# Performance work log

Measured on AMD Instinct MI355X. Metric: run time of the kernel, lower is better.

## Reference

```python
import jax, jax.numpy as jnp
import numpy as np

T, HEADS, DIM_HEAD = 16, 16, 72
M = HEADS * DIM_HEAD  # 1152
SCALE = DIM_HEAD ** -0.5


def _ln(x, eps):
    mu = x.mean(-1, keepdims=True)
    var = x.var(-1, keepdims=True)
    return (x - mu) / jnp.sqrt(var + eps)


def _rotate_half(t):
    # interleaved pairs (x1, x2) -> (-x2, x1), as in rotary-embedding-torch
    t1, t2 = t[..., 0::2], t[..., 1::2]
    return jnp.stack([-t2, t1], axis=-1).reshape(t.shape)


def _rotary(t, pos):
    d = t.shape[-1]
    inv_freq = 1.0 / (10000.0 ** (jnp.arange(0, d, 2, dtype=jnp.float32) / d))
    freqs = pos.astype(jnp.float32)[:, None] * inv_freq          # (T, d/2)
    freqs = jnp.repeat(freqs, 2, axis=-1)                        # (T, d)
    return t * jnp.cos(freqs) + _rotate_half(t) * jnp.sin(freqs)


def _forward(x, c4t, c, W_ada, b_ada, tn_w, tn_b, t_qkv, t_k, t_v, t_out,
             t_fc_w, t_fc_b, s_qkv, s_k, s_v, s_out,
             mlp_w1, mlp_b1, mlp_w2, mlp_b2, f):
    B = c4t.shape[0]
    K, N, _ = x.shape

    ada = jax.nn.silu(c4t) @ W_ada + b_ada                       # (B, 6M)
    sh_msa, sc_msa, g_msa, sh_mlp, sc_mlp, g_mlp = jnp.split(ada, 6, axis=1)

    x4 = x.reshape(B, T, N, M)

    # ---- temporal attention (seq dim = frames, rotary, per-frame cond k/v) ----
    xt = _ln(x4, 1e-5) * tn_w + tn_b                             # temporal_norm1
    xt = xt.transpose(0, 2, 1, 3)                                # (B, N, T, M)
    q, k, v = jnp.split(xt @ t_qkv, 3, axis=-1)

    def heads_t(t):  # (B,N,T,M) -> (B,N,h,T,d)
        return t.reshape(B, N, T, HEADS, DIM_HEAD).transpose(0, 1, 3, 2, 4)

    q, k, v = map(heads_t, (q, k, v))
    k = _rotary(k, f)
    ek = (c @ t_k).reshape(B, T, HEADS, DIM_HEAD).transpose(0, 2, 1, 3)  # (B,h,T,d)
    ev = (c @ t_v).reshape(B, T, HEADS, DIM_HEAD).transpose(0, 2, 1, 3)
    ek = _rotary(ek, f)
    ek = jnp.broadcast_to(ek[:, None], k.shape)                  # (B,N,h,T,d)
    ev = jnp.broadcast_to(ev[:, None], v.shape)
    kk = jnp.concatenate([ek, k], axis=-2)                       # (B,N,h,2T,d)
    vv = jnp.concatenate([ev, v], axis=-2)
    q = _rotary(q * SCALE, f)
    attn = jax.nn.softmax(jnp.einsum('bnhid,bnhjd->bnhij', q, kk), axis=-1)
    out = jnp.einsum('bnhij,bnhjd->bnhid', attn, vv)
    out = out.transpose(0, 1, 3, 2, 4).reshape(B, N, T, M) @ t_out
    res = out.transpose(0, 2, 1, 3) @ t_fc_w + t_fc_b            # (B,T,N,M)
    x4 = x4 + res

    # ---- spatial attention with adaLN modulate + one cond token per frame ----
    mod = _ln(x4, 1e-6) * (1.0 + sc_msa[:, None, None, :]) + sh_msa[:, None, None, :]
    q, k, v = jnp.split(mod @ s_qkv, 3, axis=-1)

    def heads_s(t):  # (B,T,N,M) -> (B,T,h,N,d)
        return t.reshape(B, T, N, HEADS, DIM_HEAD).transpose(0, 1, 3, 2, 4)

    q, k, v = map(heads_s, (q, k, v))
    ek = (c @ s_k).reshape(B, T, HEADS, DIM_HEAD)[:, :, :, None, :]  # (B,T,h,1,d)
    ev = (c @ s_v).reshape(B, T, HEADS, DIM_HEAD)[:, :, :, None, :]
    kk = jnp.concatenate([ek, k], axis=-2)                       # (B,T,h,N+1,d)
    vv = jnp.concatenate([ev, v], axis=-2)
    attn = jax.nn.softmax(jnp.einsum('bthid,bthjd->bthij', q * SCALE, kk), axis=-1)
    out = jnp.einsum('bthij,bthjd->bthid', attn, vv)
    out = out.transpose(0, 1, 3, 2, 4).reshape(B, T, N, M) @ s_out
    x4 = x4 + g_msa[:, None, None, :] * out

    # ---- gated MLP with adaLN modulate ----
    mod2 = _ln(x4, 1e-6) * (1.0 + sc_mlp[:, None, None, :]) + sh_mlp[:, None, None, :]
    h = jax.nn.gelu(mod2 @ mlp_w1 + mlp_b1, approximate=True)
    y = h @ mlp_w2 + mlp_b2
    x4 = x4 + g_mlp[:, None, None, :] * y
    return x4.reshape(K, N, M)


def setup_inputs() -> dict:
    key = jax.random.key(0)
    ks = jax.random.split(key, 20)
    B, N = 2, 256

    def w(k, shape, s=0.02):
        return jax.random.normal(k, shape, jnp.float32) * s

    return {
        'x': jax.random.normal(ks[0], (B * T, N, M), jnp.float32),
        'c4t': jax.random.normal(ks[1], (B, M), jnp.float32),
        'c': jax.random.normal(ks[2], (B, T, M), jnp.float32),
        'W_ada': w(ks[3], (M, 6 * M)), 'b_ada': w(ks[4], (6 * M,)),
        'tn_w': jnp.ones(M, jnp.float32), 'tn_b': jnp.zeros(M, jnp.float32),
        't_qkv': w(ks[5], (M, 3 * M)), 't_k': w(ks[6], (M, M)),
        't_v': w(ks[7], (M, M)), 't_out': w(ks[8], (M, M)),
        't_fc_w': w(ks[9], (M, M)), 't_fc_b': jnp.zeros(M, jnp.float32),
        's_qkv': w(ks[10], (M, 3 * M)), 's_k': w(ks[11], (M, M)),
        's_v': w(ks[12], (M, M)), 's_out': w(ks[13], (M, M)),
        'mlp_w1': w(ks[14], (M, 4 * M)), 'mlp_b1': jnp.zeros(4 * M, jnp.float32),
        'mlp_w2': w(ks[15], (4 * M, M)), 'mlp_b2': jnp.zeros(M, jnp.float32),
        'f': jnp.arange(T, dtype=jnp.int32),
    }


def reference(x, c4t, c, W_ada, b_ada, tn_w, tn_b, t_qkv, t_k, t_v, t_out,
              t_fc_w, t_fc_b, s_qkv, s_k, s_v, s_out,
              mlp_w1, mlp_b1, mlp_w2, mlp_b2, f):
    return _forward(x, c4t, c, W_ada, b_ada, tn_w, tn_b, t_qkv, t_k, t_v, t_out,
                    t_fc_w, t_fc_b, s_qkv, s_k, s_v, s_out,
                    mlp_w1, mlp_b1, mlp_w2, mlp_b2, f)
```

## Files before the change

### kernel.cpp

```cpp
#include <hip/hip_runtime.h>
#include <hip/hip_bf16.h>

typedef __hip_bfloat16 bf16;
typedef __attribute__((ext_vector_type(8))) short short8;
typedef __attribute__((ext_vector_type(4))) float floatx4;

__device__ __forceinline__ float b2f(bf16 v) { return __bfloat162float(v); }
__device__ __forceinline__ short f2bs(float v) {
    bf16 h = __float2bfloat16(v);
    return *(short*)&h;
}
__device__ __forceinline__ float invfreq(int jj) {
    return expf(-0.25584278811044955f * (float)jj);
}

template<int MODE>
__device__ __forceinline__ float ldin(const void* p, long i) {
    if (MODE == 0) return b2f(((const bf16*)p)[i]);
    else           return ((const float*)p)[i];
}

#define SCALE_ 0.11785113019775793f

#define GLDS(gp, lp) __builtin_amdgcn_global_load_lds( \
    (const __attribute__((address_space(1))) void*)(gp), \
    (__attribute__((address_space(3))) void*)(lp), 16, 0, 0)

__global__ void k_detect(const void* __restrict__ x, int* __restrict__ flag)
{
    const unsigned short* u = (const unsigned short*)x;
    int tid = threadIdx.x;
    int insane = 0;
    for (int i = tid; i < 2048; i += 64) {
        unsigned short s = u[i];
        int ex = (s >> 7) & 0xFF;
        if (ex >= 0xC5) insane++;
    }
    #pragma unroll
    for (int off = 32; off > 0; off >>= 1) insane += __shfl_down(insane, off);
    if (tid == 0) flag[0] = (insane > 8) ? 1 : 0;
}

__global__ void k_rope(const int* __restrict__ f, float* __restrict__ ropeC,
                       float* __restrict__ ropeS)
{
    int idx = blockIdx.x * 256 + threadIdx.x;
    if (idx < 1152) {
        int t = idx / 72, d = idx - t * 72;
        float ang = (float)f[t] * invfreq(d >> 1);
        float sn, cs; sincosf(ang, &sn, &cs);
        ropeC[idx] = cs;
        ropeS[idx] = sn;
    }
}

__global__ void k_silu(const void* __restrict__ c4t, float* __restrict__ out,
                       const int* __restrict__ flg)
{
    int i = blockIdx.x * 256 + threadIdx.x;
    if (i < 2304) {
        float v = (*flg == 0) ? ldin<0>(c4t, i) : ldin<1>(c4t, i);
        out[i] = v / (1.f + expf(-v));
    }
}

__global__ void k_cvt(const void* __restrict__ in, float* __restrict__ out, int n,
                      const int* __restrict__ flg)
{
    int i = blockIdx.x * 256 + threadIdx.x;
    if (i < n) out[i] = (*flg == 0) ? ldin<0>(in, i) : ldin<1>(in, i);
}

__global__ void k_cvtb(const float* __restrict__ in, bf16* __restrict__ out, int n)
{
    int i = blockIdx.x * 256 + threadIdx.x;
    if (i < n) out[i] = __float2bfloat16(in[i]);
}

template<int MODE>
__device__ __forceinline__ void wt_body(float (*tile)[33], const void* __restrict__ W,
    bf16* __restrict__ Wt, int K, int N)
{
    int n0 = blockIdx.x << 5, k0 = blockIdx.y << 5;
    int tid = threadIdx.x;
    int r = tid >> 3, c4 = (tid & 7) << 2;
    long base = (long)(k0 + r) * N + n0 + c4;
    #pragma unroll
    for (int i = 0; i < 4; ++i) tile[r][c4 + i] = ldin<MODE>(W, base + i);
    __syncthreads();
    long obase = (long)(n0 + r) * K + k0 + c4;
    #pragma unroll
    for (int i = 0; i < 4; ++i) Wt[obase + i] = __float2bfloat16(tile[c4 + i][r]);
}

__global__ __launch_bounds__(256) void k_wt(const void* __restrict__ W,
    bf16* __restrict__ Wt, int K, int N, const int* __restrict__ flg)
{
    __shared__ float tile[32][33];
    if (*flg == 0) wt_body<0>(tile, W, Wt, K, N);
    else           wt_body<1>(tile, W, Wt, K, N);
}

template<int MODE>
__device__ __forceinline__ void gemm_body(
    float (*As)[64], float (*Bs)[64],
    const float* __restrict__ A, const void* __restrict__ W,
    const void* __restrict__ bias, float* __restrict__ C,
    int R, int K, int N)
{
    int tid = threadIdx.x;
    int tx = tid & 15, ty = tid >> 4;
    int row0 = blockIdx.y << 6;
    int col0 = blockIdx.x << 6;
    float acc[4][4] = {};
    int ar = tid >> 2;
    int ak = (tid & 3) << 2;
    int bk = tid >> 4;
    int bc = (tid & 15) << 2;
    for (int kt = 0; kt < K; kt += 16) {
        if (row0 + ar < R) {
            const float4 a4 = *(const float4*)(A + (long)(row0 + ar) * K + kt + ak);
            As[ak + 0][ar] = a4.x; As[ak + 1][ar] = a4.y;
            As[ak + 2][ar] = a4.z; As[ak + 3][ar] = a4.w;
        } else {
            As[ak + 0][ar] = 0.f; As[ak + 1][ar] = 0.f;
            As[ak + 2][ar] = 0.f; As[ak + 3][ar] = 0.f;
        }
        #pragma unroll
        for (int i = 0; i < 4; ++i)
            Bs[bk][bc + i] = ldin<MODE>(W, (long)(kt + bk) * N + col0 + bc + i);
        __syncthreads();
        #pragma unroll
        for (int kk = 0; kk < 16; ++kk) {
            float4 av = *(const float4*)&As[kk][ty << 2];
            float4 bv = *(const float4*)&Bs[kk][tx << 2];
            float a[4] = {av.x, av.y, av.z, av.w};
            float b[4] = {bv.x, bv.y, bv.z, bv.w};
            #pragma unroll
            for (int i = 0; i < 4; ++i)
                #pragma unroll
                for (int j = 0; j < 4; ++j)
                    acc[i][j] += a[i] * b[j];
        }
        __syncthreads();
    }
    #pragma unroll
    for (int i = 0; i < 4; ++i) {
        int gr = row0 + (ty << 2) + i;
        if (gr >= R) continue;
        float* cp = C + (long)gr * N + col0 + (tx << 2);
        #pragma unroll
        for (int j = 0; j < 4; ++j) {
            float v = acc[i][j];
            if (bias) v += ldin<MODE>(bias, col0 + (tx << 2) + j);
            cp[j] = v;
        }
    }
}

__global__ __launch_bounds__(256) void k_gemm(
    const float* __restrict__ A, const void* __restrict__ W,
    const void* __restrict__ bias, float* __restrict__ C,
    int R, int K, int N, const int* __restrict__ flg)
{
    __shared__ float As[16][64];
    __shared__ float Bs[16][64];
    if (*flg == 0) gemm_body<0>(As, Bs, A, W, bias, C, R, K, N);
    else           gemm_body<1>(As, Bs, A, W, bias, C, R, K, N);
}

template<int EMODE>
__global__ __launch_bounds__(256) void k_mgemm(
    const bf16* __restrict__ A, const bf16* __restrict__ Wt,
    const float* __restrict__ bias, void* __restrict__ Cout,
    int K, int N, int outbf, int act,
    float* __restrict__ x4, const float* __restrict__ ada, int part,
    const void* __restrict__ xin, void* __restrict__ outp,
    const int* __restrict__ flg)
{
    __shared__ short As[8192];
    __shared__ short Bs[8192];
    int tid = threadIdx.x;
    int lane = tid & 63, wave = tid >> 6;
    int mq = wave >> 1, nq = wave & 1;

    int gx = gridDim.x;
    int nwg = gx * (int)gridDim.y;
    int orig = blockIdx.y * gx + blockIdx.x;
    int qq = nwg >> 3, rr = nwg & 7;
    int xcd = orig & 7, loc = orig >> 3;
    int wg = (xcd < rr ? xcd * (qq + 1) : rr * (qq + 1) + (xcd - rr) * qq) + loc;
    int bx = wg % gx, by = wg / gx;

    long row0 = (long)by << 7;
    long col0 = (long)bx << 7;
    int mi = lane & 15, q = lane >> 4;

    const bf16* gA0 = A  + (row0 + (2 * wave) * 16 + mi) * K + q * 8;
    const bf16* gA1 = A  + (row0 + (2 * wave + 1) * 16 + mi) * K + q * 8;
    const bf16* gB0 = Wt + (col0 + (2 * wave) * 16 + mi) * K + q * 8;
    const bf16* gB1 = Wt + (col0 + (2 * wave + 1) * 16 + mi) * K + q * 8;
    int la0 = (2 * wave) << 9;
    int la1 = (2 * wave + 1) << 9;

    floatx4 acc[4][4] = {};

    int nt = K >> 5;
    GLDS(gA0, &As[la0]);
    GLDS(gA1, &As[la1]);
    GLDS(gB0, &Bs[la0]);
    GLDS(gB1, &Bs[la1]);
    __syncthreads();

    for (int t = 0; t < nt - 1; ++t) {
        int cur = (t & 1) << 12, nxt = cur ^ 4096;
        int kt2 = (t + 1) << 5;
        GLDS(gA0 + kt2, &As[nxt + la0]);
        GLDS(gA1 + kt2, &As[nxt + la1]);
        GLDS(gB0 + kt2, &Bs[nxt + la0]);
        GLDS(gB1 + kt2, &Bs[nxt + la1]);
        short8 af[4], bfr[4];
        #pragma unroll
        for (int i = 0; i < 4; ++i)
            af[i] = *(const short8*)&As[cur + ((4 * mq + i) << 9) + lane * 8];
        #pragma unroll
        for (int j = 0; j < 4; ++j)
            bfr[j] = *(const short8*)&Bs[cur + ((4 * nq + j) << 9) + lane * 8];
        #pragma unroll
        for (int i = 0; i < 4; ++i)
            #pragma unroll
            for (int j = 0; j < 4; ++j)
                acc[i][j] = __builtin_amdgcn_mfma_f32_16x16x32_bf16(
                    af[i], bfr[j], acc[i][j], 0, 0, 0);
        __syncthreads();
    }
    {
        int cur = ((nt - 1) & 1) << 12;
        short8 af[4], bfr[4];
        #pragma unroll
        for (int i = 0; i < 4; ++i)
            af[i] = *(const short8*)&As[cur + ((4 * mq + i) << 9) + lane * 8];
        #pragma unroll
        for (int j = 0; j < 4; ++j)
            bfr[j] = *(const short8*)&Bs[cur + ((4 * nq + j) << 9) + lane * 8];
        #pragma unroll
        for (int i = 0; i < 4; ++i)
            #pragma unroll
            for (int j = 0; j < 4; ++j)
                acc[i][j] = __builtin_amdgcn_mfma_f32_16x16x32_bf16(
                    af[i], bfr[j], acc[i][j], 0, 0, 0);
    }

    int lr = lane >> 4, lc = lane & 15;
    int fl = flg ? *flg : 0;
    float b4[4] = {0.f, 0.f, 0.f, 0.f};
    if (bias) {
        #pragma unroll
        for (int j = 0; j < 4; ++j) b4[j] = bias[(int)col0 + nq * 64 + j * 16 + lc];
    }
    #pragma unroll
    for (int i = 0; i < 4; ++i) {
        #pragma unroll
        for (int r = 0; r < 4; ++r) {
            long grow = row0 + mq * 64 + i * 16 + lr * 4 + r;
            #pragma unroll
            for (int j = 0; j < 4; ++j) {
                int col = (int)col0 + nq * 64 + j * 16 + lc;
                float v = acc[i][j][r] + b4[j];
                if (act) {
                    float u = v;
                    float tt = 1.5957691216057308f * (u + 0.044715f * u * u * u);
                    v = u / (1.f + __expf(-tt));
                }
                if constexpr (EMODE == 0) {
                    if (outbf) ((bf16*)Cout)[grow * N + col] = __float2bfloat16(v);
                    else       ((float*)Cout)[grow * N + col] = v;
                } else if constexpr (EMODE == 1) {
                    int bb = (int)(grow >> 12);
                    int nn = ((int)grow >> 4) & 255;
                    int tt2 = (int)grow & 15;
                    long rx = ((long)((bb << 4) + tt2) << 8) + nn;
                    long idx = rx * 1152 + col;
                    float xv = (fl == 0) ? b2f(((const bf16*)xin)[idx])
                                         : ((const float*)xin)[idx];
                    x4[idx] = xv + v;
                } else {
                    int bb = (int)(grow >> 12);
                    float g = ada[(bb * 6 + part) * 1152 + col];
                    long idx = grow * 1152 + col;
                    float nv = x4[idx] + g * v;
                    x4[idx] = nv;
                    if (outp) {
                        if (fl == 0) ((bf16*)outp)[idx] = __float2bfloat16(nv);
                        else         ((float*)outp)[idx] = nv;
                    }
                }
            }
        }
    }
}

template<int MODE>
__device__ __forceinline__ void ln_t_body(float* rs, float* rss,
    const void* __restrict__ x, const void* __restrict__ w,
    const void* __restrict__ bb, bf16* __restrict__ out)
{
    int r = blockIdx.x;
    int n = r & 255;
    int bt = r >> 8;
    int b = bt >> 4, t = bt & 15;
    long orow = (long)((b << 8) + n) * 16 + t;
    int tid = threadIdx.x;
    float vals[5];
    float s = 0.f, ss = 0.f;
    int c = 0;
    for (int i = tid; i < 1152; i += 256, ++c) {
        float v = ldin<MODE>(x, (long)r * 1152 + i);
        vals[c] = v; s += v; ss += v * v;
    }
    #pragma unroll
    for (int off = 32; off > 0; off >>= 1) {
        s  += __shfl_down(s, off);
        ss += __shfl_down(ss, off);
    }
    int wid = tid >> 6;
    if ((tid & 63) == 0) { rs[wid] = s; rss[wid] = ss; }
    __syncthreads();
    float S  = rs[0] + rs[1] + rs[2] + rs[3];
    float SS = rss[0] + rss[1] + rss[2] + rss[3];
    float mu = S * (1.f / 1152.f);
    float var = SS * (1.f / 1152.f) - mu * mu;
    float rstd = rsqrtf(var + 1e-5f);
    c = 0;
    bf16* op = out + orow * 1152;
    for (int i = tid; i < 1152; i += 256, ++c)
        op[i] = __float2bfloat16((vals[c] - mu) * rstd * ldin<MODE>(w, i) + ldin<MODE>(bb, i));
}

__global__ __launch_bounds__(256) void k_ln_t(
    const void* __restrict__ x, const void* __restrict__ w,
    const void* __restrict__ bb, bf16* __restrict__ out,
    const int* __restrict__ flg)
{
    __shared__ float rs[4], rss[4];
    if (*flg == 0) ln_t_body<0>(rs, rss, x, w, bb, out);
    else           ln_t_body<1>(rs, rss, x, w, bb, out);
}

__global__ __launch_bounds__(256) void k_ln_mod(
    const float* __restrict__ x4, const float* __restrict__ ada,
    int psh, int psc, float eps, bf16* __restrict__ out)
{
    int r = blockIdx.x;
    int b = r >> 12;
    const float* xp = x4 + (long)r * 1152;
    int tid = threadIdx.x;
    float vals[5];
    float s = 0.f, ss = 0.f;
    int c = 0;
    for (int i = tid; i < 1152; i += 256, ++c) {
        float v = xp[i];
        vals[c] = v; s += v; ss += v * v;
    }
    #pragma unroll
    for (int off = 32; off > 0; off >>= 1) {
        s  += __shfl_down(s, off);
        ss += __shfl_down(ss, off);
    }
    __shared__ float rs[4], rss[4];
    int wid = tid >> 6;
    if ((tid & 63) == 0) { rs[wid] = s; rss[wid] = ss; }
    __syncthreads();
    float S  = rs[0] + rs[1] + rs[2] + rs[3];
    float SS = rss[0] + rss[1] + rss[2] + rss[3];
    float mu = S * (1.f / 1152.f);
    float var = SS * (1.f / 1152.f) - mu * mu;
    float rstd = rsqrtf(var + eps);
    const float* sh = ada + (b * 6 + psh) * 1152;
    const float* sc = ada + (b * 6 + psc) * 1152;
    c = 0;
    bf16* op = out + (long)r * 1152;
    for (int i = tid; i < 1152; i += 256, ++c)
        op[i] = __float2bfloat16((vals[c] - mu) * rstd * (1.f + sc[i]) + sh[i]);
}

__global__ __launch_bounds__(256) void k_attn_t(
    const bf16* __restrict__ qkv, const float* __restrict__ ekt,
    const float* __restrict__ evt, const float* __restrict__ ropeC,
    const float* __restrict__ ropeS, bf16* __restrict__ out)
{
    __shared__ float qs[16][73];
    __shared__ float ksT[72][33];
    __shared__ float vs[32][73];
    __shared__ float sc[16][33];
    int blk = blockIdx.x;
    int h = blk & 15;
    int bn = blk >> 4;
    int b = bn >> 8;
    int tid = threadIdx.x;
    long qbase = (long)bn * 16 * 3456 + h * 72;
    for (int idx = tid; idx < 16 * 72; idx += 256) {
        int i = idx / 72, d = idx - i * 72;
        long p0 = qbase + (long)i * 3456;
        float v  = b2f(qkv[p0 + d]);
        float v2 = b2f(qkv[p0 + (d ^ 1)]);
        float cs = ropeC[idx], sn = ropeS[idx];
        float rv = (d & 1) ? (v * cs + v2 * sn) : (v * cs - v2 * sn);
        qs[i][d] = rv * SCALE_;
    }
    for (int idx = tid; idx < 32 * 72; idx += 256) {
        int j = idx / 72, d = idx - j * 72;
        float kv, kv2, vv; int pi;
        if (j < 16) {
            long base = (long)(b * 16 + j) * 1152 + h * 72;
            kv  = ekt[base + d];
            kv2 = ekt[base + (d ^ 1)];
            vv  = evt[base + d];
            pi = j;
        } else {
            int jj = j - 16;
            long base = qbase + (long)jj * 3456;
            kv  = b2f(qkv[base + 1152 + d]);
            kv2 = b2f(qkv[base + 1152 + (d ^ 1)]);
            vv  = b2f(qkv[base + 2304 + d]);
            pi = jj;
        }
        float cs = ropeC[pi * 72 + d], sn = ropeS[pi * 72 + d];
        ksT[d][j] = (d & 1) ? (kv * cs + kv2 * sn) : (kv * cs - kv2 * sn);
        vs[j][d] = vv;
    }
    __syncthreads();
    for (int e = tid; e < 512; e += 256) {
        int i = e >> 5, j = e & 31;
        float s = 0.f;
        for (int d = 0; d < 72; ++d) s += qs[i][d] * ksT[d][j];
        sc[i][j] = s;
    }
    __syncthreads();
    if (tid < 16) {
        float m = -1e30f;
        for (int j = 0; j < 32; ++j) m = fmaxf(m, sc[tid][j]);
        float l = 0.f;
        for (int j = 0; j < 32; ++j) { float p = expf(sc[tid][j] - m); sc[tid][j] = p; l += p; }
        float inv = 1.f / l;
        for (int j = 0; j < 32; ++j) sc[tid][j] *= inv;
    }
    __syncthreads();
    for (int idx = tid; idx < 16 * 72; idx += 256) {
        int i = idx / 72, d = idx - i * 72;
        float o = 0.f;
        for (int j = 0; j < 32; ++j) o += sc[i][j] * vs[j][d];
        out[((long)bn * 16 + i) * 1152 + h * 72 + d] = __float2bfloat16(o);
    }
}

__global__ __launch_bounds__(256) void k_attn_s(
    const bf16* __restrict__ qkv, const bf16* __restrict__ eksb,
    const bf16* __restrict__ evsb, bf16* __restrict__ out)
{
    __shared__ short vT[5120];
    __shared__ short pl[4][1024];
    int tid = threadIdx.x;
    int lane = tid & 63, wave = tid >> 6;
    int blk = blockIdx.x;
    int ic = blk & 3;
    int bth = blk >> 2;
    int h = bth & 15;
    int bt = bth >> 4;
    int col = lane & 15, q = lane >> 4;
    int hoff = h * 72;
    long qkvbase = (long)bt * 256 * 3456;
    long ctxbase = (long)bt * 1152 + hoff;

    int qrow = ic * 64 + wave * 16 + col;
    const bf16* qptr = qkv + qkvbase + (long)qrow * 3456 + hoff;
    short8 qf[3];
    #pragma unroll
    for (int ks = 0; ks < 3; ++ks) {
        int k0 = ks * 32 + q * 8;
        if (k0 + 8 <= 72) qf[ks] = *(const short8*)(qptr + k0);
        else { short8 z = {0,0,0,0,0,0,0,0}; qf[ks] = z; }
    }

    floatx4 o[5] = {};
    float m_i[4], l_i[4];
    #pragma unroll
    for (int r = 0; r < 4; ++r) { m_i[r] = -1e30f; l_i[r] = 0.f; }

    for (int kc = 0; kc < 320; kc += 64) {
        for (int fi = tid; fi < 640; fi += 256) {
            int blkid = fi >> 6, fl2 = fi & 63;
            int dn = blkid >> 1, ks = blkid & 1;
            int d = dn * 16 + (fl2 & 15);
            int kq = fl2 >> 4;
            short8 v;
            #pragma unroll
            for (int j = 0; j < 8; ++j) {
                int gk = kc + ks * 32 + kq * 8 + j;
                short sv = 0;
                if (d < 72 && gk <= 256) {
                    if (gk == 0) sv = *(const short*)(eksb ? &evsb[ctxbase + d] : nullptr);
                    else sv = *(const short*)&qkv[qkvbase + (long)(gk - 1) * 3456 + 2304 + hoff + d];
                }
                v[j] = sv;
            }
            *(short8*)&vT[blkid * 512 + fl2 * 8] = v;
        }
        __syncthreads();

        floatx4 sacc[4] = {};
        #pragma unroll
        for (int nt = 0; nt < 4; ++nt) {
            int key = kc + nt * 16 + col;
            #pragma unroll
            for (int ks = 0; ks < 3; ++ks) {
                int k0 = ks * 32 + q * 8;
                short8 kf = {0,0,0,0,0,0,0,0};
                if (key <= 256 && k0 + 8 <= 72) {
                    if (key == 0) kf = *(const short8*)(eksb + ctxbase + k0);
                    else kf = *(const short8*)(qkv + qkvbase + (long)(key - 1) * 3456 + 1152 + hoff + k0);
                }
                sacc[nt] = __builtin_amdgcn_mfma_f32_16x16x32_bf16(qf[ks], kf, sacc[nt], 0, 0, 0);
            }
        }

        float p[4][4];
        #pragma unroll
        for (int r = 0; r < 4; ++r) {
            float mv = -1e30f;
            #pragma unroll
            for (int nt = 0; nt < 4; ++nt) {
                int key = kc + nt * 16 + col;
                float s = (key <= 256) ? sacc[nt][r] * SCALE_ : -1e30f;
                p[nt][r] = s;
                mv = fmaxf(mv, s);
            }
            #pragma unroll
            for (int xm = 1; xm < 16; xm <<= 1) mv = fmaxf(mv, __shfl_xor(mv, xm));
            float mn = fmaxf(m_i[r], mv);
            float alpha = expf(m_i[r] - mn);
            m_i[r] = mn;
            float rsum = 0.f;
            #pragma unroll
            for (int nt = 0; nt < 4; ++nt) {
                float e = expf(p[nt][r] - mn);
                p[nt][r] = e;
                rsum += e;
            }
            #pragma unroll
            for (int xm = 1; xm < 16; xm <<= 1) rsum += __shfl_xor(rsum, xm);
            l_i[r] = l_i[r] * alpha + rsum;
            #pragma unroll
            for (int dn = 0; dn < 5; ++dn) o[dn][r] *= alpha;
        }

        #pragma unroll
        for (int nt = 0; nt < 4; ++nt) {
            int kl = nt * 16 + col;
            int ks2 = kl >> 5, q2 = (kl >> 3) & 3, j = kl & 7;
            #pragma unroll
            for (int r = 0; r < 4; ++r) {
                int mrow = q * 4 + r;
                pl[wave][ks2 * 512 + q2 * 128 + mrow * 8 + j] = f2bs(p[nt][r]);
            }
        }
        __syncthreads();

        #pragma unroll
        for (int ks = 0; ks < 2; ++ks) {
            short8 pf = *(const short8*)&pl[wave][ks * 512 + lane * 8];
            #pragma unroll
            for (int dn = 0; dn < 5; ++dn) {
                short8 vf = *(const short8*)&vT[(dn * 2 + ks) * 512 + lane * 8];
                o[dn] = __builtin_amdgcn_mfma_f32_16x16x32_bf16(pf, vf, o[dn], 0, 0, 0);
            }
        }
        __syncthreads();
    }

    int orow0 = ic * 64 + wave * 16;
    #pragma unroll
    for (int dn = 0; dn < 5; ++dn) {
        int d = dn * 16 + col;
        if (d >= 72) continue;
        #pragma unroll
        for (int r = 0; r < 4; ++r) {
            int mrow = q * 4 + r;
            float val = o[dn][r] / l_i[r];
            out[((long)bt * 256 + orow0 + mrow) * 1152 + hoff + d] = __float2bfloat16(val);
        }
    }
}

extern "C" void kernel_launch(void* const* d_in, const int* in_sizes, int n_in,
                              void* d_out, int out_size, void* d_ws, size_t ws_size,
                              hipStream_t stream)
{
    const void* x      = d_in[0];
    const void* c4t    = d_in[1];
    const void* c      = d_in[2];
    const void* W_ada  = d_in[3];
    const void* b_ada  = d_in[4];
    const void* tn_w   = d_in[5];
    const void* tn_b   = d_in[6];
    const void* t_qkv  = d_in[7];
    const void* t_k    = d_in[8];
    const void* t_v    = d_in[9];
    const void* t_outw = d_in[10];
    const void* t_fcw  = d_in[11];
    const void* t_fcb  = d_in[12];
    const void* s_qkv  = d_in[13];
    const void* s_k    = d_in[14];
    const void* s_v    = d_in[15];
    const void* s_outw = d_in[16];
    const void* mlp_w1 = d_in[17];
    const void* mlp_b1 = d_in[18];
    const void* mlp_w2 = d_in[19];
    const void* mlp_b2 = d_in[20];
    const int*  f      = (const int*)d_in[21];

    float* ws    = (float*)d_ws;
    float* x4    = ws;
    float* buf2  = x4 + 9437184;
    float* reg1f = buf2 + 9437184;
    bf16*  qkvb  = (bf16*)reg1f;
    bf16*  hbf   = (bf16*)reg1f;
    float* abfAf = reg1f + 18874368;
    bf16*  abfA  = (bf16*)abfAf;
    float* abfBf = abfAf + 4718592;
    bf16*  abfB  = (bf16*)abfBf;
    float* wtf   = abfBf + 4718592;
    bf16*  wt    = (bf16*)wtf;
    bf16* t_qkv_t = wt;
    bf16* s_qkv_t = t_qkv_t + 3981312;
    bf16* t_out_t = s_qkv_t + 3981312;
    bf16* t_fc_t  = t_out_t + 1327104;
    bf16* s_out_t = t_fc_t  + 1327104;
    bf16* w1_t    = s_out_t + 1327104;
    bf16* w2_t    = w1_t    + 5308416;
    float* small  = wtf + 11280384;
    float* ada   = small;
    float* cf32  = ada  + 13824;
    float* ekt   = cf32 + 36864;
    float* evt   = ekt  + 36864;
    float* eks   = evt  + 36864;
    float* evs   = eks  + 36864;
    bf16*  eksb  = (bf16*)(evs + 36864);
    bf16*  evsb  = eksb + 36864;
    float* sc4   = (float*)(evsb + 36864);
    float* fcb_f = sc4  + 2304;
    float* b1_f  = fcb_f + 1152;
    float* b2_f  = b1_f  + 4608;
    float* ropeC = b2_f + 1152;
    float* ropeS = ropeC + 1152;
    int*   flg   = (int*)(ropeS + 1152);

    k_detect<<<1, 64, 0, stream>>>(x, flg);
    k_rope<<<5, 256, 0, stream>>>(f, ropeC, ropeS);

    k_silu<<<9, 256, 0, stream>>>(c4t, sc4, flg);
    k_gemm<<<dim3(108, 1), 256, 0, stream>>>(sc4, W_ada, b_ada, ada, 2, 1152, 6912, flg);

    k_cvt<<<144, 256, 0, stream>>>(c, cf32, 36864, flg);
    k_gemm<<<dim3(18, 1), 256, 0, stream>>>(cf32, t_k, nullptr, ekt, 32, 1152, 1152, flg);
    k_gemm<<<dim3(18, 1), 256, 0, stream>>>(cf32, t_v, nullptr, evt, 32, 1152, 1152, flg);
    k_gemm<<<dim3(18, 1), 256, 0, stream>>>(cf32, s_k, nullptr, eks, 32, 1152, 1152, flg);
    k_gemm<<<dim3(18, 1), 256, 0, stream>>>(cf32, s_v, nullptr, evs, 32, 1152, 1152, flg);
    k_cvtb<<<144, 256, 0, stream>>>(eks, eksb, 36864);
    k_cvtb<<<144, 256, 0, stream>>>(evs, evsb, 36864);

    k_cvt<<<5, 256, 0, stream>>>(t_fcb, fcb_f, 1152, flg);
    k_cvt<<<18, 256, 0, stream>>>(mlp_b1, b1_f, 4608, flg);
    k_cvt<<<5, 256, 0, stream>>>(mlp_b2, b2_f, 1152, flg);

    k_wt<<<dim3(108, 36), 256, 0, stream>>>(t_qkv, t_qkv_t, 1152, 3456, flg);
    k_wt<<<dim3(108, 36), 256, 0, stream>>>(s_qkv, s_qkv_t, 1152, 3456, flg);
    k_wt<<<dim3(36, 36), 256, 0, stream>>>(t_outw, t_out_t, 1152, 1152, flg);
    k_wt<<<dim3(36, 36), 256, 0, stream>>>(t_fcw, t_fc_t, 1152, 1152, flg);
    k_wt<<<dim3(36, 36), 256, 0, stream>>>(s_outw, s_out_t, 1152, 1152, flg);
    k_wt<<<dim3(144, 36), 256, 0, stream>>>(mlp_w1, w1_t, 1152, 4608, flg);
    k_wt<<<dim3(36, 144), 256, 0, stream>>>(mlp_w2, w2_t, 4608, 1152, flg);

    k_ln_t<<<8192, 256, 0, stream>>>(x, tn_w, tn_b, abfA, flg);
    k_mgemm<0><<<dim3(27, 64), 256, 0, stream>>>(abfA, t_qkv_t, nullptr, qkvb, 1152, 3456, 1, 0,
                                                 nullptr, nullptr, 0, nullptr, nullptr, flg);
    k_attn_t<<<8192, 256, 0, stream>>>(qkvb, ekt, evt, ropeC, ropeS, abfB);
    k_mgemm<0><<<dim3(9, 64), 256, 0, stream>>>(abfB, t_out_t, nullptr, abfA, 1152, 1152, 1, 0,
                                                nullptr, nullptr, 0, nullptr, nullptr, flg);
    k_mgemm<1><<<dim3(9, 64), 256, 0, stream>>>(abfA, t_fc_t, fcb_f, nullptr, 1152, 1152, 0, 0,
                                                x4, nullptr, 0, x, nullptr, flg);

    k_ln_mod<<<8192, 256, 0, stream>>>(x4, ada, 0, 1, 1e-6f, abfA);
    k_mgemm<0><<<dim3(27, 64), 256, 0, stream>>>(abfA, s_qkv_t, nullptr, qkvb, 1152, 3456, 1, 0,
                                                 nullptr, nullptr, 0, nullptr, nullptr, flg);
    k_attn_s<<<2048, 256, 0, stream>>>(qkvb, eksb, evsb, abfB);
    k_mgemm<2><<<dim3(9, 64), 256, 0, stream>>>(abfB, s_out_t, nullptr, nullptr, 1152, 1152, 0, 0,
                                                x4, ada, 2, nullptr, nullptr, flg);

    k_ln_mod<<<8192, 256, 0, stream>>>(x4, ada, 3, 4, 1e-6f, abfA);
    k_mgemm<0><<<dim3(36, 64), 256, 0, stream>>>(abfA, w1_t, b1_f, hbf, 1152, 4608, 1, 1,
                                                 nullptr, nullptr, 0, nullptr, nullptr, flg);
    k_mgemm<2><<<dim3(9, 64), 256, 0, stream>>>(hbf, w2_t, b2_f, nullptr, 4608, 1152, 0, 0,
                                                x4, ada, 5, nullptr, d_out, flg);
}
```

Measured before the change: 1.724 ms.

## Enlarge GEMM tile to 256x128 with 8 waves and triple-buffered LDS pipeline

```diff
diff --git a/kernel.cpp b/kernel.cpp
--- a/kernel.cpp
+++ b/kernel.cpp
@@ -170,7 +170,7 @@
 }
 
 template<int EMODE>
-__global__ __launch_bounds__(256) void k_mgemm(
+__global__ __launch_bounds__(512, 4) void k_mgemm(
     const bf16* __restrict__ A, const bf16* __restrict__ Wt,
     const float* __restrict__ bias, void* __restrict__ Cout,
     int K, int N, int outbf, int act,
@@ -178,11 +178,11 @@
     const void* __restrict__ xin, void* __restrict__ outp,
     const int* __restrict__ flg)
 {
-    __shared__ short As[8192];
-    __shared__ short Bs[8192];
+    __shared__ short As[24576];
+    __shared__ short Bs[12288];
     int tid = threadIdx.x;
     int lane = tid & 63, wave = tid >> 6;
-    int mq = wave >> 1, nq = wave & 1;
+    int wm = wave >> 1, wn = wave & 1;
 
     int gx = gridDim.x;
     int nwg = gx * (int)gridDim.y;
@@ -192,63 +192,69 @@
     int wg = (xcd < rr ? xcd * (qq + 1) : rr * (qq + 1) + (xcd - rr) * qq) + loc;
     int bx = wg % gx, by = wg / gx;
 
-    long row0 = (long)by << 7;
+    long row0 = (long)by << 8;
     long col0 = (long)bx << 7;
     int mi = lane & 15, q = lane >> 4;
 
     const bf16* gA0 = A  + (row0 + (2 * wave) * 16 + mi) * K + q * 8;
-    const bf16* gA1 = A  + (row0 + (2 * wave + 1) * 16 + mi) * K + q * 8;
-    const bf16* gB0 = Wt + (col0 + (2 * wave) * 16 + mi) * K + q * 8;
-    const bf16* gB1 = Wt + (col0 + (2 * wave + 1) * 16 + mi) * K + q * 8;
-    int la0 = (2 * wave) << 9;
-    int la1 = (2 * wave + 1) << 9;
+    const bf16* gA1 = gA0 + 16 * K;
+    const bf16* gB0 = Wt + (col0 + wave * 16 + mi) * K + q * 8;
+    int dA0 = (2 * wave) * 512, dA1 = (2 * wave + 1) * 512, dB0 = wave * 512;
 
     floatx4 acc[4][4] = {};
-
     int nt = K >> 5;
-    GLDS(gA0, &As[la0]);
-    GLDS(gA1, &As[la1]);
-    GLDS(gB0, &Bs[la0]);
-    GLDS(gB1, &Bs[la1]);
-    __syncthreads();
-
-    for (int t = 0; t < nt - 1; ++t) {
-        int cur = (t & 1) << 12, nxt = cur ^ 4096;
-        int kt2 = (t + 1) << 5;
-        GLDS(gA0 + kt2, &As[nxt + la0]);
-        GLDS(gA1 + kt2, &As[nxt + la1]);
-        GLDS(gB0 + kt2, &Bs[nxt + la0]);
-        GLDS(gB1 + kt2, &Bs[nxt + la1]);
-        short8 af[4], bfr[4];
-        #pragma unroll
-        for (int i = 0; i < 4; ++i)
-            af[i] = *(const short8*)&As[cur + ((4 * mq + i) << 9) + lane * 8];
-        #pragma unroll
-        for (int j = 0; j < 4; ++j)
-            bfr[j] = *(const short8*)&Bs[cur + ((4 * nq + j) << 9) + lane * 8];
-        #pragma unroll
-        for (int i = 0; i < 4; ++i)
+
+    GLDS(gA0,      &As[dA0]);
+    GLDS(gA1,      &As[dA1]);
+    GLDS(gB0,      &Bs[dB0]);
+    GLDS(gA0 + 32, &As[8192 + dA0]);
+    GLDS(gA1 + 32, &As[8192 + dA1]);
+    GLDS(gB0 + 32, &Bs[4096 + dB0]);
+    __builtin_amdgcn_sched_barrier(0);
+    asm volatile("s_waitcnt vmcnt(3)" ::: "memory");
+    __builtin_amdgcn_sched_barrier(0);
+    __builtin_amdgcn_s_barrier();
+    __builtin_amdgcn_sched_barrier(0);
+
+    int aRd = wm * 2048 + lane * 8;
+    int bRd = wn * 2048 + lane * 8;
+    int cs = 0;
+    int si = 2;
+
+    for (int t = 0; t < nt; ++t) {
+        if (t + 2 < nt) {
+            int oA = si << 13, oB = si << 12;
+            int kt2 = (t + 2) << 5;
+            GLDS(gA0 + kt2, &As[oA + dA0]);
+            GLDS(gA1 + kt2, &As[oA + dA1]);
+            GLDS(gB0 + kt2, &Bs[oB + dB0]);
+        }
+        {
+            int oA = cs << 13, oB = cs << 12;
+            short8 af[4], bfr[4];
+            #pragma unroll
+            for (int i = 0; i < 4; ++i)
+                af[i] = *(const short8*)&As[oA + aRd + i * 512];
             #pragma unroll
             for (int j = 0; j < 4; ++j)
-                acc[i][j] = __builtin_amdgcn_mfma_f32_16x16x32_bf16(
-                    af[i], bfr[j], acc[i][j], 0, 0, 0);
-        __syncthreads();
-    }
-    {
-        int cur = ((nt - 1) & 1) << 12;
-        short8 af[4], bfr[4];
-        #pragma unroll
-        for (int i = 0; i < 4; ++i)
-            af[i] = *(const short8*)&As[cur + ((4 * mq + i) << 9) + lane * 8];
-        #pragma unroll
-        for (int j = 0; j < 4; ++j)
-            bfr[j] = *(const short8*)&Bs[cur + ((4 * nq + j) << 9) + lane * 8];
-        #pragma unroll
-        for (int i = 0; i < 4; ++i)
-            #pragma unroll
-            for (int j = 0; j < 4; ++j)
-                acc[i][j] = __builtin_amdgcn_mfma_f32_16x16x32_bf16(
-                    af[i], bfr[j], acc[i][j], 0, 0, 0);
+                bfr[j] = *(const short8*)&Bs[oB + bRd + j * 512];
+            #pragma unroll
+            for (int i = 0; i < 4; ++i)
+                #pragma unroll
+                for (int j = 0; j < 4; ++j)
+                    acc[i][j] = __builtin_amdgcn_mfma_f32_16x16x32_bf16(
+                        af[i], bfr[j], acc[i][j], 0, 0, 0);
+        }
+        __builtin_amdgcn_sched_barrier(0);
+        if (t + 2 < nt) asm volatile("s_waitcnt vmcnt(3)" ::: "memory");
+        else            asm volatile("s_waitcnt vmcnt(0)" ::: "memory");
+        __builtin_amdgcn_sched_barrier(0);
+        if (t < nt - 1) {
+            __builtin_amdgcn_s_barrier();
+            __builtin_amdgcn_sched_barrier(0);
+        }
+        cs = (cs == 2) ? 0 : cs + 1;
+        si = (si == 2) ? 0 : si + 1;
     }
 
     int lr = lane >> 4, lc = lane & 15;
@@ -256,16 +262,16 @@
     float b4[4] = {0.f, 0.f, 0.f, 0.f};
     if (bias) {
         #pragma unroll
-        for (int j = 0; j < 4; ++j) b4[j] = bias[(int)col0 + nq * 64 + j * 16 + lc];
+        for (int j = 0; j < 4; ++j) b4[j] = bias[(int)col0 + wn * 64 + j * 16 + lc];
     }
     #pragma unroll
     for (int i = 0; i < 4; ++i) {
         #pragma unroll
         for (int r = 0; r < 4; ++r) {
-            long grow = row0 + mq * 64 + i * 16 + lr * 4 + r;
+            long grow = row0 + wm * 64 + i * 16 + lr * 4 + r;
             #pragma unroll
             for (int j = 0; j < 4; ++j) {
-                int col = (int)col0 + nq * 64 + j * 16 + lc;
+                int col = (int)col0 + wn * 64 + j * 16 + lc;
                 float v = acc[i][j][r] + b4[j];
                 if (act) {
                     float u = v;
@@ -682,24 +688,24 @@
     k_wt<<<dim3(36, 144), 256, 0, stream>>>(mlp_w2, w2_t, 4608, 1152, flg);
 
     k_ln_t<<<8192, 256, 0, stream>>>(x, tn_w, tn_b, abfA, flg);
-    k_mgemm<0><<<dim3(27, 64), 256, 0, stream>>>(abfA, t_qkv_t, nullptr, qkvb, 1152, 3456, 1, 0,
+    k_mgemm<0><<<dim3(27, 32), 512, 0, stream>>>(abfA, t_qkv_t, nullptr, qkvb, 1152, 3456, 1, 0,
                                                  nullptr, nullptr, 0, nullptr, nullptr, flg);
     k_attn_t<<<8192, 256, 0, stream>>>(qkvb, ekt, evt, ropeC, ropeS, abfB);
-    k_mgemm<0><<<dim3(9, 64), 256, 0, stream>>>(abfB, t_out_t, nullptr, abfA, 1152, 1152, 1, 0,
+    k_mgemm<0><<<dim3(9, 32), 512, 0, stream>>>(abfB, t_out_t, nullptr, abfA, 1152, 1152, 1, 0,
                                                 nullptr, nullptr, 0, nullptr, nullptr, flg);
-    k_mgemm<1><<<dim3(9, 64), 256, 0, stream>>>(abfA, t_fc_t, fcb_f, nullptr, 1152, 1152, 0, 0,
+    k_mgemm<1><<<dim3(9, 32), 512, 0, stream>>>(abfA, t_fc_t, fcb_f, nullptr, 1152, 1152, 0, 0,
                                                 x4, nullptr, 0, x, nullptr, flg);
 
     k_ln_mod<<<8192, 256, 0, stream>>>(x4, ada, 0, 1, 1e-6f, abfA);
-    k_mgemm<0><<<dim3(27, 64), 256, 0, stream>>>(abfA, s_qkv_t, nullptr, qkvb, 1152, 3456, 1, 0,
+    k_mgemm<0><<<dim3(27, 32), 512, 0, stream>>>(abfA, s_qkv_t, nullptr, qkvb, 1152, 3456, 1, 0,
                                                  nullptr, nullptr, 0, nullptr, nullptr, flg);
     k_attn_s<<<2048, 256, 0, stream>>>(qkvb, eksb, evsb, abfB);
-    k_mgemm<2><<<dim3(9, 64), 256, 0, stream>>>(abfB, s_out_t, nullptr, nullptr, 1152, 1152, 0, 0,
+    k_mgemm<2><<<dim3(9, 32), 512, 0, stream>>>(abfB, s_out_t, nullptr, nullptr, 1152, 1152, 0, 0,
                                                 x4, ada, 2, nullptr, nullptr, flg);
 
     k_ln_mod<<<8192, 256, 0, stream>>>(x4, ada, 3, 4, 1e-6f, abfA);
-    k_mgemm<0><<<dim3(36, 64), 256, 0, stream>>>(abfA, w1_t, b1_f, hbf, 1152, 4608, 1, 1,
+    k_mgemm<0><<<dim3(36, 32), 512, 0, stream>>>(abfA, w1_t, b1_f, hbf, 1152, 4608, 1, 1,
                                                  nullptr, nullptr, 0, nullptr, nullptr, flg);
-    k_mgemm<2><<<dim3(9, 64), 256, 0, stream>>>(hbf, w2_t, b2_f, nullptr, 4608, 1152, 0, 0,
+    k_mgemm<2><<<dim3(9, 32), 512, 0, stream>>>(hbf, w2_t, b2_f, nullptr, 4608, 1152, 0, 0,
                                                 x4, ada, 5, nullptr, d_out, flg);
 }
```

Measured after the change: 1.683 ms. 1.02x faster.
